# Performance work log

Measured on AMD Instinct MI355X. Metric: run time of the kernel, lower is better.

Reference implementation:

```python
import jax, jax.numpy as jnp
import numpy as np

Z_DIM = 64
C_DIM = 4
HIDDEN = 128
N_NODES = 50000
N_EDGES = 1600000
BN_EPS = 1e-5


def setup_inputs() -> dict:
    key = jax.random.key(0)
    ks = jax.random.split(key, 12)
    in_dim = 2 * Z_DIM + C_DIM
    def lin_init(k, fan_in, shape):
        bound = 1.0 / np.sqrt(fan_in)
        return jax.random.uniform(k, shape, jnp.float32, -bound, bound)
    return {
        "z": jax.random.normal(ks[0], (N_NODES, Z_DIM), jnp.float32),
        "edge_index": jax.random.randint(ks[1], (2, N_EDGES), 0, N_NODES, jnp.int64),
        "c": jax.random.normal(ks[2], (C_DIM,), jnp.float32),
        "W1": lin_init(ks[3], in_dim, (in_dim, HIDDEN)),
        "b1": lin_init(ks[4], in_dim, (HIDDEN,)),
        "gamma": jnp.ones((HIDDEN,), jnp.float32),
        "beta": jnp.zeros((HIDDEN,), jnp.float32),
        "W2": lin_init(ks[5], HIDDEN, (HIDDEN, HIDDEN)),
        "b2": lin_init(ks[6], HIDDEN, (HIDDEN,)),
        "W3": lin_init(ks[7], HIDDEN, (HIDDEN, 1)),
        "b3": lin_init(ks[8], HIDDEN, (1,)),
    }


def reference(z, edge_index, c, W1, b1, gamma, beta, W2, b2, W3, b3):
    src, dst = edge_index[0], edge_index[1]
    E = src.shape[0]
    # [E, 2*z_dim + c_dim]: gather both endpoints, broadcast condition
    pairs = jnp.concatenate(
        [z[src], z[dst], jnp.broadcast_to(c[None, :], (E, c.shape[0]))], axis=-1
    )
    h = jax.nn.relu(pairs @ W1 + b1)
    # BatchNorm1d (training mode: batch statistics, biased variance)
    mean = jnp.mean(h, axis=0)
    var = jnp.var(h, axis=0)
    h = (h - mean) * jax.lax.rsqrt(var + BN_EPS) * gamma + beta
    h = jax.nn.relu(h @ W2 + b2)
    logits = (h @ W3 + b3).squeeze(-1)  # [E]
    return logits
```

## Files before the change

kernel.cpp:

```cpp
#include <hip/hip_runtime.h>
#include <stdint.h>

typedef _Float16 f16x8 __attribute__((ext_vector_type(8)));
typedef float    f32x4 __attribute__((ext_vector_type(4)));
typedef unsigned u32x4 __attribute__((ext_vector_type(4)));

union Frag { u32x4 q; f16x8 h; unsigned u[4]; };

static __device__ __forceinline__ unsigned short f2h(float f) {
  _Float16 h = (_Float16)f;
  return __builtin_bit_cast(unsigned short, h);
}
static __device__ __forceinline__ void dec4i(unsigned a, unsigned b, int* h) {
  unsigned lo = (a & 0x00FF00FFu) + (b & 0x00FF00FFu);
  unsigned hi = ((a >> 8) & 0x00FF00FFu) + ((b >> 8) & 0x00FF00FFu);
  int t0 = (int)(lo & 0xFFFFu) - 256;
  int t1 = (int)(hi & 0xFFFFu) - 256;
  int t2 = (int)(lo >> 16) - 256;
  int t3 = (int)(hi >> 16) - 256;
  h[0] = t0 > 0 ? t0 : 0; h[1] = t1 > 0 ? t1 : 0;
  h[2] = t2 > 0 ? t2 : 0; h[3] = t3 > 0 ? t3 : 0;
}
static __device__ __forceinline__ void mg2(unsigned y, unsigned& w0, unsigned& w1) {
  w0 = (y & 0x00FF00FFu) + 0x64006400u;
  w1 = ((y >> 8) & 0x00FF00FFu) + 0x64006400u;
}
template<int CTRL>
static __device__ __forceinline__ float dppadd(float s) {
  int v = __builtin_amdgcn_mov_dpp(__builtin_bit_cast(int, s), CTRL, 0xf, 0xf, true);
  return s + __builtin_bit_cast(float, v);
}

__global__ __launch_bounds__(256) void k_nodeproj(
    const float* __restrict__ z, const float* __restrict__ c,
    const float* __restrict__ W1, const float* __restrict__ b1,
    unsigned* __restrict__ gmax1, unsigned* __restrict__ gmax2,
    float* __restrict__ Tf1, float* __restrict__ Tf2, int n_nodes) {
  __shared__ float zl[128 * 64];
  const int t = threadIdx.x;
  const int j = t & 127;
  const int half = t >> 7;
  const int nb = blockIdx.x * 128;
  {
    const float* zsrc = z + (size_t)nb * 64;
    const int limit = (n_nodes - nb) * 64;
    for (int i = t; i < 2048; i += 256) {
      f32x4 v = {0.f, 0.f, 0.f, 0.f};
      if (i * 4 + 3 < limit) {
        v = *(const f32x4*)(zsrc + i * 4);
      } else {
        #pragma unroll
        for (int q = 0; q < 4; ++q) if (i * 4 + q < limit) v[q] = zsrc[i * 4 + q];
      }
      *(f32x4*)(zl + i * 4) = v;
    }
  }
  float kvj = b1[j];
  #pragma unroll
  for (int q = 0; q < 4; ++q) kvj += c[q] * W1[(128 + q) * 128 + j];
  __syncthreads();

  float wreg[64];
  #pragma unroll
  for (int d = 0; d < 64; ++d) wreg[d] = W1[d * 128 + j];
  float mx = 0.f;
  for (int i = 0; i < 64; ++i) {
    const int n = i * 2 + half;
    const int gn = nb + n;
    float acc = kvj;
    #pragma unroll
    for (int d4 = 0; d4 < 16; ++d4) {
      f32x4 zz = *(const f32x4*)(zl + n * 64 + d4 * 4);
      acc += zz[0]*wreg[d4*4+0] + zz[1]*wreg[d4*4+1]
           + zz[2]*wreg[d4*4+2] + zz[3]*wreg[d4*4+3];
    }
    if (gn < n_nodes) {
      Tf1[(size_t)gn * 128 + j] = acc;
      mx = fmaxf(mx, fabsf(acc));
    }
  }
  atomicMax(&gmax1[j], __float_as_uint(mx));
  #pragma unroll
  for (int d = 0; d < 64; ++d) wreg[d] = W1[(64 + d) * 128 + j];
  mx = 0.f;
  for (int i = 0; i < 64; ++i) {
    const int n = i * 2 + half;
    const int gn = nb + n;
    float acc = 0.f;
    #pragma unroll
    for (int d4 = 0; d4 < 16; ++d4) {
      f32x4 zz = *(const f32x4*)(zl + n * 64 + d4 * 4);
      acc += zz[0]*wreg[d4*4+0] + zz[1]*wreg[d4*4+1]
           + zz[2]*wreg[d4*4+2] + zz[3]*wreg[d4*4+3];
    }
    if (gn < n_nodes) {
      Tf2[(size_t)gn * 128 + j] = acc;
      mx = fmaxf(mx, fabsf(acc));
    }
  }
  atomicMax(&gmax2[j], __float_as_uint(mx));
}

__global__ __launch_bounds__(256) void k_quant(
    const float* __restrict__ Tf1, const float* __restrict__ Tf2,
    const unsigned* __restrict__ g1, const unsigned* __restrict__ g2,
    unsigned char* __restrict__ U1, unsigned char* __restrict__ U2,
    int n_nodes) {
  const int tid = blockIdx.x * 256 + threadIdx.x;
  const int tot = n_nodes * 8;
  if (tid >= 2 * tot) return;
  const int table = tid >= tot;
  const int r = tid - table * tot;
  const int node = r >> 3, g = r & 7;
  const float* src = (table ? Tf2 : Tf1) + (size_t)node * 128 + g * 16;
  unsigned char* dst = (table ? U2 : U1) + (size_t)node * 128;
  f32x4 v[4];
  #pragma unroll
  for (int q = 0; q < 4; ++q) v[q] = *(const f32x4*)(src + q * 4);
  #pragma unroll
  for (int b = 0; b < 2; ++b) {
    unsigned w0 = 0, w1 = 0;
    #pragma unroll
    for (int k = 0; k < 8; ++k) {
      const int f = g * 16 + b * 8 + k;
      float m = fmaxf(fmaxf(__uint_as_float(g1[f]), __uint_as_float(g2[f])),
                      1e-20f);
      float dij = 127.0f / m;
      float acc = v[b * 2 + (k >> 2)][k & 3];
      int q8 = (int)rintf(acc * dij);
      q8 = q8 > 127 ? 127 : (q8 < -127 ? -127 : q8);
      unsigned by = (unsigned)(q8 + 128);
      if (k < 4) w0 |= by << (8 * k); else w1 |= by << (8 * (k - 4));
    }
    const int off = (((2 * g + b) & 3) * 32) + ((g >> 1) * 8);
    *(unsigned*)(dst + off)     = w0;
    *(unsigned*)(dst + off + 4) = w1;
  }
}

template<int WH8>
__global__ __launch_bounds__(512) void k_stats(
    const int* __restrict__ ei, const unsigned char* __restrict__ U1,
    const unsigned char* __restrict__ U2,
    unsigned long long* __restrict__ gstat,
    unsigned char* __restrict__ H8, int E, int niter16) {
  __shared__ int red[8][256];
  const int t = threadIdx.x;
  const int w = t >> 6, l = t & 63;
  const int es = l >> 3, ch = l & 7;
  int sm[16], sq[16];
  #pragma unroll
  for (int k = 0; k < 16; ++k) { sm[k] = 0; sq[k] = 0; }
  const int nw = gridDim.x * 8;
  int itc = blockIdx.x * 8 + w;
  int itn = itc + nw;
  u32x4 a0c, b0c, a1c, b1c, a0n, b0n, a1n, b1n;
  int ns0 = 0, nd0 = 0, ns1 = 0, nd1 = 0;
  if (itc < niter16) {
    const int e = itc * 16;
    int s0 = ei[e + es],     d0 = ei[E + e + es];
    int s1 = ei[e + 8 + es], d1 = ei[E + e + 8 + es];
    a0c = *(const u32x4*)(U1 + (size_t)s0 * 128 + ch * 16);
    b0c = *(const u32x4*)(U2 + (size_t)d0 * 128 + ch * 16);
    a1c = *(const u32x4*)(U1 + (size_t)s1 * 128 + ch * 16);
    b1c = *(const u32x4*)(U2 + (size_t)d1 * 128 + ch * 16);
  }
  if (itn < niter16) {
    const int e = itn * 16;
    ns0 = ei[e + es];     nd0 = ei[E + e + es];
    ns1 = ei[e + 8 + es]; nd1 = ei[E + e + 8 + es];
  }
  while (itc < niter16) {
    const bool vn = itn < niter16;
    if (vn) {
      a0n = *(const u32x4*)(U1 + (size_t)ns0 * 128 + ch * 16);
      b0n = *(const u32x4*)(U2 + (size_t)nd0 * 128 + ch * 16);
      a1n = *(const u32x4*)(U1 + (size_t)ns1 * 128 + ch * 16);
      b1n = *(const u32x4*)(U2 + (size_t)nd1 * 128 + ch * 16);
      const int it2 = itn + nw;
      if (it2 < niter16) {
        const int e = it2 * 16;
        ns0 = ei[e + es];     nd0 = ei[E + e + es];
        ns1 = ei[e + 8 + es]; nd1 = ei[E + e + 8 + es];
      }
    }
    const int e16 = itc * 16;
    u32x4 o0, o1;
    #pragma unroll
    for (int qq = 0; qq < 4; ++qq) {
      int h[4];
      dec4i(a0c[qq], b0c[qq], h);
      #pragma unroll
      for (int r = 0; r < 4; ++r) { sm[qq*4+r] += h[r]; sq[qq*4+r] += h[r]*h[r]; }
      if (WH8) o0[qq] = (unsigned)h[0] | ((unsigned)h[2] << 8)
                      | ((unsigned)h[1] << 16) | ((unsigned)h[3] << 24);
      dec4i(a1c[qq], b1c[qq], h);
      #pragma unroll
      for (int r = 0; r < 4; ++r) { sm[qq*4+r] += h[r]; sq[qq*4+r] += h[r]*h[r]; }
      if (WH8) o1[qq] = (unsigned)h[0] | ((unsigned)h[2] << 8)
                      | ((unsigned)h[1] << 16) | ((unsigned)h[3] << 24);
    }
    if (WH8) {
      *(u32x4*)(H8 + (size_t)(e16 + es) * 128 + ch * 16)     = o0;
      *(u32x4*)(H8 + (size_t)(e16 + 8 + es) * 128 + ch * 16) = o1;
    }
    if (!vn) break;
    a0c = a0n; b0c = b0n; a1c = a1n; b1c = b1n;
    itc = itn; itn += nw;
  }
  #pragma unroll
  for (int k = 0; k < 16; ++k) {
    sm[k] += __shfl_xor(sm[k], 8, 64);
    sm[k] += __shfl_xor(sm[k], 16, 64);
    sm[k] += __shfl_xor(sm[k], 32, 64);
    sq[k] += __shfl_xor(sq[k], 8, 64);
    sq[k] += __shfl_xor(sq[k], 16, 64);
    sq[k] += __shfl_xor(sq[k], 32, 64);
  }
  if (es == 0) {
    #pragma unroll
    for (int k = 0; k < 16; ++k) {
      int f = ((ch & 1) * 2 + (k >> 3)) * 32 + (ch >> 1) * 8 + (k & 7);
      red[w][f]       = sm[k];
      red[w][128 + f] = sq[k];
    }
  }
  __syncthreads();
  if (t < 256) {
    long long s = 0;
    #pragma unroll
    for (int ww = 0; ww < 8; ++ww) s += red[ww][t];
    atomicAdd(&gstat[t], (unsigned long long)s);
  }
}

__global__ __launch_bounds__(1024) void k_finalize(
    const unsigned long long* __restrict__ gstat,
    const float* __restrict__ gamma, const float* __restrict__ beta,
    const float* __restrict__ W2, const float* __restrict__ b2,
    const unsigned* __restrict__ gmax1, const unsigned* __restrict__ gmax2,
    unsigned short* __restrict__ W2t, float* __restrict__ b2p,
    float* __restrict__ b2ps, double Einv) {
  __shared__ float ajd[128], bbj[128];
  __shared__ float bacc[8][128];
  const int t = threadIdx.x;
  if (t < 128) {
    float m = fmaxf(fmaxf(__uint_as_float(gmax1[t]), __uint_as_float(gmax2[t])),
                    1e-20f);
    double d8 = (double)(m * (1.0f / 127.0f));
    double mean = d8 * (double)gstat[t] * Einv;
    double ex2  = d8 * d8 * (double)gstat[128 + t] * Einv;
    double var  = ex2 - mean * mean;
    float a = (float)((double)gamma[t] / sqrt(var + 1e-5));
    ajd[t] = a * (float)d8;
    bbj[t] = beta[t] - (float)mean * a;
  }
  __syncthreads();
  for (int cidx = t; cidx < 16384; cidx += 1024) {
    int i = cidx >> 7;
    int j = cidx & 127;
    W2t[j * 128 + i] = f2h(ajd[i] * W2[cidx]);
  }
  {
    const int col = t & 127, g2 = t >> 7;
    float acc = 0.f;
    #pragma unroll
    for (int q = 0; q < 16; ++q) {
      int i = g2 * 16 + q;
      acc += bbj[i] * W2[i * 128 + col];
    }
    bacc[g2][col] = acc;
  }
  __syncthreads();
  if (t < 128) {
    float a = b2[t];
    #pragma unroll
    for (int g3 = 0; g3 < 8; ++g3) a += bacc[g3][t];
    b2p[t] = a;
    float c = 0.f;
    for (int i = 0; i < 128; ++i)
      c += (float)((_Float16)(ajd[i] * W2[i * 128 + t]));
    b2ps[t] = a - 1024.0f * c;
  }
}

__global__ __launch_bounds__(256) void k_edge_h8(
    const unsigned char* __restrict__ H8, const unsigned short* __restrict__ W2t,
    const float* __restrict__ b2ps, const float* __restrict__ W3,
    const float* __restrict__ b3, float* __restrict__ out, int ntiles) {
  const int t = threadIdx.x;
  const int w = t >> 6, l = t & 63;
  const int lm = l & 15, lg = l >> 4;
  const int lo32 = lg * 32;
  Frag Bf[8][4];
  #pragma unroll
  for (int nt = 0; nt < 8; ++nt)
    #pragma unroll
    for (int s = 0; s < 4; ++s)
      Bf[nt][s].q = *(const u32x4*)((const char*)W2t +
                      (size_t)(nt*16 + lm) * 256 + s*64 + lg*16);
  float b2r[8], w3r[8];
  #pragma unroll
  for (int nt = 0; nt < 8; ++nt) {
    b2r[nt] = b2ps[nt*16 + lm];
    w3r[nt] = W3[nt*16 + lm];
  }
  const float b3v = *b3;
  const int stride = gridDim.x;
  int tile = blockIdx.x;
  if (tile >= ntiles) return;
  int ebase = tile*64 + w*16;
  u32x4 Y0, Y1, N0, N1;
  {
    const unsigned char* r0 = H8 + (size_t)(ebase + lm) * 128 + lo32;
    Y0 = *(const u32x4*)r0;  Y1 = *(const u32x4*)(r0 + 16);
  }
  while (true) {
    const int next = tile + stride;
    const bool has_next = next < ntiles;
    const int pref = has_next ? next : tile;
    const int neb = pref*64 + w*16;
    {
      const unsigned char* n0 = H8 + (size_t)(neb + lm) * 128 + lo32;
      N0 = *(const u32x4*)n0;  N1 = *(const u32x4*)(n0 + 16);
    }
    f32x4 acc[8];
    #pragma unroll
    for (int nt = 0; nt < 8; ++nt) {
      f32x4 zed = {0.f, 0.f, 0.f, 0.f};
      acc[nt] = zed;
    }
    Frag fa;
    #define MFMAS(S)                                                        \
      _Pragma("unroll")                                                     \
      for (int nt = 0; nt < 8; ++nt)                                        \
        acc[nt] = __builtin_amdgcn_mfma_f32_16x16x32_f16(fa.h, Bf[nt][S].h, \
                                                         acc[nt], 0, 0, 0);
    mg2(Y0[0], fa.u[0], fa.u[1]); mg2(Y0[1], fa.u[2], fa.u[3]);
    MFMAS(0)
    mg2(Y0[2], fa.u[0], fa.u[1]); mg2(Y0[3], fa.u[2], fa.u[3]);
    MFMAS(1)
    mg2(Y1[0], fa.u[0], fa.u[1]); mg2(Y1[1], fa.u[2], fa.u[3]);
    MFMAS(2)
    mg2(Y1[2], fa.u[0], fa.u[1]); mg2(Y1[3], fa.u[2], fa.u[3]);
    MFMAS(3)
    #undef MFMAS
    #pragma unroll
    for (int r = 0; r < 4; ++r) {
      float sum = 0.f;
      #pragma unroll
      for (int nt = 0; nt < 8; ++nt) {
        float h2 = fmaxf(acc[nt][r] + b2r[nt], 0.f);
        sum += h2 * w3r[nt];
      }
      sum = dppadd<0xB1>(sum);
      sum = dppadd<0x4E>(sum);
      sum += __shfl_xor(sum, 4, 64);
      sum += __shfl_xor(sum, 8, 64);
      if (lm == 0) out[ebase + lg*4 + r] = sum + b3v;
    }
    if (!has_next) break;
    tile = next;
    ebase = neb;
    Y0 = N0;  Y1 = N1;
  }
}

extern "C" void kernel_launch(void* const* d_in, const int* in_sizes, int n_in,
                              void* d_out, int out_size, void* d_ws, size_t ws_size,
                              hipStream_t stream) {
  const float* z     = (const float*)d_in[0];
  const int*   ei    = (const int*)d_in[1];
  const float* c     = (const float*)d_in[2];
  const float* W1    = (const float*)d_in[3];
  const float* b1    = (const float*)d_in[4];
  const float* gamma = (const float*)d_in[5];
  const float* beta  = (const float*)d_in[6];
  const float* W2    = (const float*)d_in[7];
  const float* b2    = (const float*)d_in[8];
  const float* W3    = (const float*)d_in[9];
  const float* b3    = (const float*)d_in[10];
  float* out = (float*)d_out;

  const int n_nodes = in_sizes[0] / 64;
  const int E       = in_sizes[1] / 2;
  const int NB2 = 1024;

  char* ws = (char*)d_ws;
  const size_t nb128 = (size_t)n_nodes * 128;
  unsigned char* U1 = (unsigned char*)ws;
  unsigned char* U2 = U1 + nb128;
  char* p = (char*)(U2 + nb128);
  unsigned short* W2t = (unsigned short*)p;      p += 32768;
  float* b2p          = (float*)p;               p += 512;
  float* b2ps         = (float*)p;               p += 512;
  unsigned* gmax1     = (unsigned*)p;            p += 512;
  unsigned* gmax2     = (unsigned*)p;            p += 512;
  unsigned long long* gstat = (unsigned long long*)p;  p += 2048;
  unsigned char* H8   = (unsigned char*)p;
  float* Tf1 = (float*)H8;
  float* Tf2 = Tf1 + (size_t)n_nodes * 128;
  const size_t need = (size_t)((char*)H8 - ws) + (size_t)E * 128;
  const bool use_h8 = (ws_size >= need);

  (void)hipMemsetAsync(gmax1, 0, 3072, stream);
  const int npb = (n_nodes + 127) / 128;
  k_nodeproj<<<npb, 256, 0, stream>>>(z, c, W1, b1, gmax1, gmax2,
                                      Tf1, Tf2, n_nodes);
  const int nqb = (n_nodes * 16 + 255) / 256;
  k_quant<<<nqb, 256, 0, stream>>>(Tf1, Tf2, gmax1, gmax2, U1, U2, n_nodes);
  if (use_h8)
    k_stats<1><<<NB2, 512, 0, stream>>>(ei, U1, U2, gstat, H8, E, E/16);
  else
    k_stats<0><<<NB2, 512, 0, stream>>>(ei, U1, U2, gstat, H8, E, E/16);
  k_finalize<<<1, 1024, 0, stream>>>(gstat, gamma, beta, W2, b2,
                                     gmax1, gmax2, W2t, b2p, b2ps,
                                     1.0 / (double)E);
  k_edge_h8<<<512, 256, 0, stream>>>(H8, W2t, b2ps, W3, b3, out, E/64);
}
```

Baseline: 272.6 us.

## Compute node projection with fp16 MFMA and prepacked W1 fragments

```diff
diff --git a/kernel.cpp b/kernel.cpp
--- a/kernel.cpp
+++ b/kernel.cpp
@@ -10,6 +10,12 @@
 static __device__ __forceinline__ unsigned short f2h(float f) {
   _Float16 h = (_Float16)f;
   return __builtin_bit_cast(unsigned short, h);
+}
+static __device__ __forceinline__ unsigned packhf(float lo, float hi) {
+  _Float16 a = (_Float16)lo, b = (_Float16)hi;
+  unsigned short x = __builtin_bit_cast(unsigned short, a);
+  unsigned short y = __builtin_bit_cast(unsigned short, b);
+  return (unsigned)x | ((unsigned)y << 16);
 }
 static __device__ __forceinline__ void dec4i(unsigned a, unsigned b, int* h) {
   unsigned lo = (a & 0x00FF00FFu) + (b & 0x00FF00FFu);
@@ -31,74 +37,94 @@
   return s + __builtin_bit_cast(float, v);
 }
 
-__global__ __launch_bounds__(256) void k_nodeproj(
-    const float* __restrict__ z, const float* __restrict__ c,
+__global__ __launch_bounds__(256) void k_wprep(
     const float* __restrict__ W1, const float* __restrict__ b1,
+    const float* __restrict__ c, unsigned short* __restrict__ W1h,
+    float* __restrict__ kvbuf) {
+  const int e = blockIdx.x * 256 + threadIdx.x;
+  const int frag = e >> 6, lane = e & 63;
+  const int h = frag >> 4, ks = (frag >> 3) & 1, nt = frag & 7;
+  const int lm = lane & 15, lg = lane >> 4;
+  u32x4 ov;
+  #pragma unroll
+  for (int p = 0; p < 4; ++p) {
+    unsigned short s0 = f2h(W1[(size_t)(h*64 + ks*32 + lg*8 + 2*p)     * 128 + nt*16 + lm]);
+    unsigned short s1 = f2h(W1[(size_t)(h*64 + ks*32 + lg*8 + 2*p + 1) * 128 + nt*16 + lm]);
+    ov[p] = (unsigned)s0 | ((unsigned)s1 << 16);
+  }
+  *(u32x4*)(W1h + (size_t)e * 8) = ov;
+  if (blockIdx.x == 0 && threadIdx.x < 128) {
+    const int f = threadIdx.x;
+    float kv = b1[f];
+    #pragma unroll
+    for (int q = 0; q < 4; ++q) kv += c[q] * W1[(128 + q) * 128 + f];
+    kvbuf[f] = kv;
+  }
+}
+
+__global__ __launch_bounds__(256) void k_npmfma(
+    const float* __restrict__ z, const unsigned short* __restrict__ W1h,
+    const float* __restrict__ kvbuf,
     unsigned* __restrict__ gmax1, unsigned* __restrict__ gmax2,
-    float* __restrict__ Tf1, float* __restrict__ Tf2, int n_nodes) {
-  __shared__ float zl[128 * 64];
+    float* __restrict__ Tf1, float* __restrict__ Tf2, int ntiles16) {
+  __shared__ unsigned lmx[2][128];
   const int t = threadIdx.x;
-  const int j = t & 127;
-  const int half = t >> 7;
-  const int nb = blockIdx.x * 128;
-  {
-    const float* zsrc = z + (size_t)nb * 64;
-    const int limit = (n_nodes - nb) * 64;
-    for (int i = t; i < 2048; i += 256) {
-      f32x4 v = {0.f, 0.f, 0.f, 0.f};
-      if (i * 4 + 3 < limit) {
-        v = *(const f32x4*)(zsrc + i * 4);
-      } else {
+  if (t < 256) ((unsigned*)lmx)[t] = 0u;
+  __syncthreads();
+  const int w = t >> 6, l = t & 63;
+  const int lm = l & 15, lg = l >> 4;
+  const int tile = blockIdx.x * 4 + w;
+  if (tile < ntiles16) {
+    const int mbase = tile * 16;
+    Frag A0, A1;
+    {
+      const float* zr = z + (size_t)(mbase + lm) * 64 + lg * 8;
+      f32x4 v0 = *(const f32x4*)zr;
+      f32x4 v1 = *(const f32x4*)(zr + 4);
+      f32x4 v2 = *(const f32x4*)(zr + 32);
+      f32x4 v3 = *(const f32x4*)(zr + 36);
+      A0.u[0] = packhf(v0[0], v0[1]); A0.u[1] = packhf(v0[2], v0[3]);
+      A0.u[2] = packhf(v1[0], v1[1]); A0.u[3] = packhf(v1[2], v1[3]);
+      A1.u[0] = packhf(v2[0], v2[1]); A1.u[1] = packhf(v2[2], v2[3]);
+      A1.u[2] = packhf(v3[0], v3[1]); A1.u[3] = packhf(v3[2], v3[3]);
+    }
+    #pragma unroll
+    for (int h = 0; h < 2; ++h) {
+      Frag Bf[2][8];
+      #pragma unroll
+      for (int ks = 0; ks < 2; ++ks)
         #pragma unroll
-        for (int q = 0; q < 4; ++q) if (i * 4 + q < limit) v[q] = zsrc[i * 4 + q];
+        for (int nt = 0; nt < 8; ++nt)
+          Bf[ks][nt].q = *(const u32x4*)(W1h +
+              ((size_t)(h*16 + ks*8 + nt) * 64 + l) * 8);
+      f32x4 acc[8];
+      #pragma unroll
+      for (int nt = 0; nt < 8; ++nt) {
+        float iv = h ? 0.f : kvbuf[nt * 16 + lm];
+        f32x4 z4 = {iv, iv, iv, iv};
+        acc[nt] = z4;
       }
-      *(f32x4*)(zl + i * 4) = v;
-    }
-  }
-  float kvj = b1[j];
-  #pragma unroll
-  for (int q = 0; q < 4; ++q) kvj += c[q] * W1[(128 + q) * 128 + j];
+      #pragma unroll
+      for (int nt = 0; nt < 8; ++nt) {
+        acc[nt] = __builtin_amdgcn_mfma_f32_16x16x32_f16(A0.h, Bf[0][nt].h, acc[nt], 0, 0, 0);
+        acc[nt] = __builtin_amdgcn_mfma_f32_16x16x32_f16(A1.h, Bf[1][nt].h, acc[nt], 0, 0, 0);
+      }
+      float* Tf = h ? Tf2 : Tf1;
+      #pragma unroll
+      for (int nt = 0; nt < 8; ++nt) {
+        float m = fmaxf(fmaxf(fabsf(acc[nt][0]), fabsf(acc[nt][1])),
+                        fmaxf(fabsf(acc[nt][2]), fabsf(acc[nt][3])));
+        atomicMax(&lmx[h][nt*16 + lm], __float_as_uint(m));
+        #pragma unroll
+        for (int r = 0; r < 4; ++r)
+          __builtin_nontemporal_store(acc[nt][r],
+              Tf + (size_t)(mbase + lg*4 + r) * 128 + nt*16 + lm);
+      }
+    }
+  }
   __syncthreads();
-
-  float wreg[64];
-  #pragma unroll
-  for (int d = 0; d < 64; ++d) wreg[d] = W1[d * 128 + j];
-  float mx = 0.f;
-  for (int i = 0; i < 64; ++i) {
-    const int n = i * 2 + half;
-    const int gn = nb + n;
-    float acc = kvj;
-    #pragma unroll
-    for (int d4 = 0; d4 < 16; ++d4) {
-      f32x4 zz = *(const f32x4*)(zl + n * 64 + d4 * 4);
-      acc += zz[0]*wreg[d4*4+0] + zz[1]*wreg[d4*4+1]
-           + zz[2]*wreg[d4*4+2] + zz[3]*wreg[d4*4+3];
-    }
-    if (gn < n_nodes) {
-      Tf1[(size_t)gn * 128 + j] = acc;
-      mx = fmaxf(mx, fabsf(acc));
-    }
-  }
-  atomicMax(&gmax1[j], __float_as_uint(mx));
-  #pragma unroll
-  for (int d = 0; d < 64; ++d) wreg[d] = W1[(64 + d) * 128 + j];
-  mx = 0.f;
-  for (int i = 0; i < 64; ++i) {
-    const int n = i * 2 + half;
-    const int gn = nb + n;
-    float acc = 0.f;
-    #pragma unroll
-    for (int d4 = 0; d4 < 16; ++d4) {
-      f32x4 zz = *(const f32x4*)(zl + n * 64 + d4 * 4);
-      acc += zz[0]*wreg[d4*4+0] + zz[1]*wreg[d4*4+1]
-           + zz[2]*wreg[d4*4+2] + zz[3]*wreg[d4*4+3];
-    }
-    if (gn < n_nodes) {
-      Tf2[(size_t)gn * 128 + j] = acc;
-      mx = fmaxf(mx, fabsf(acc));
-    }
-  }
-  atomicMax(&gmax2[j], __float_as_uint(mx));
+  if (t < 128) atomicMax(&gmax1[t], lmx[0][t]);
+  else         atomicMax(&gmax2[t - 128], lmx[1][t - 128]);
 }
 
 __global__ __launch_bounds__(256) void k_quant(
@@ -116,7 +142,8 @@
   unsigned char* dst = (table ? U2 : U1) + (size_t)node * 128;
   f32x4 v[4];
   #pragma unroll
-  for (int q = 0; q < 4; ++q) v[q] = *(const f32x4*)(src + q * 4);
+  for (int q = 0; q < 4; ++q)
+    v[q] = __builtin_nontemporal_load((const f32x4*)(src + q * 4));
   #pragma unroll
   for (int b = 0; b < 2; ++b) {
     unsigned w0 = 0, w1 = 0;
@@ -392,6 +419,8 @@
   unsigned char* U2 = U1 + nb128;
   char* p = (char*)(U2 + nb128);
   unsigned short* W2t = (unsigned short*)p;      p += 32768;
+  unsigned short* W1h = (unsigned short*)p;      p += 32768;
+  float* kvbuf        = (float*)p;               p += 512;
   float* b2p          = (float*)p;               p += 512;
   float* b2ps         = (float*)p;               p += 512;
   unsigned* gmax1     = (unsigned*)p;            p += 512;
@@ -404,9 +433,10 @@
   const bool use_h8 = (ws_size >= need);
 
   (void)hipMemsetAsync(gmax1, 0, 3072, stream);
-  const int npb = (n_nodes + 127) / 128;
-  k_nodeproj<<<npb, 256, 0, stream>>>(z, c, W1, b1, gmax1, gmax2,
-                                      Tf1, Tf2, n_nodes);
+  k_wprep<<<8, 256, 0, stream>>>(W1, b1, c, W1h, kvbuf);
+  const int ntiles16 = n_nodes / 16;
+  k_npmfma<<<(ntiles16 + 3) / 4, 256, 0, stream>>>(z, W1h, kvbuf, gmax1, gmax2,
+                                                   Tf1, Tf2, ntiles16);
   const int nqb = (n_nodes * 16 + 255) / 256;
   k_quant<<<nqb, 256, 0, stream>>>(Tf1, Tf2, gmax1, gmax2, U1, U2, n_nodes);
   if (use_h8)
```

New measurement: 234.6 us, median of 2. 1.16x faster.
